# Kernel optimization log

Hardware: AMD Instinct MI355X
Metric: run time of the kernel (lower is better)

## Reference

```python
import jax, jax.numpy as jnp
import numpy as np

N_WIN = 7    # n_win hardcoded in AR_Attention
TOPK = 4     # topk routing windows
HEADS = 8    # num_heads


def setup_inputs() -> dict:
    key = jax.random.key(0)
    ks = jax.random.split(key, 6)
    B, H, W, C = 4, 56, 56, 256
    s = 0.02
    x = jax.random.normal(ks[0], (B, H, W, C), jnp.float32)
    Wqkv = jax.random.normal(ks[1], (C, 3 * C), jnp.float32) * s  # Linear(dim, 3*dim) (qk_dim=dim)
    bqkv = jnp.zeros((3 * C,), jnp.float32)
    Wo = jax.random.normal(ks[2], (C, C), jnp.float32) * s        # output projection Linear(dim, dim)
    bo = jnp.zeros((C,), jnp.float32)
    lepe_w = jax.random.normal(ks[3], (5, 5, 1, C), jnp.float32) * s  # 5x5 depthwise conv (side_dwconv=5)
    lepe_b = jnp.zeros((C,), jnp.float32)
    return {"x": x, "Wqkv": Wqkv, "bqkv": bqkv, "Wo": Wo, "bo": bo,
            "lepe_w": lepe_w, "lepe_b": lepe_b}


def reference(x, Wqkv, bqkv, Wo, bo, lepe_w, lepe_b):
    B, H, W, C = x.shape
    nw = N_WIN
    h, w = H // nw, W // nw           # region size (8x8)
    p2 = nw * nw                      # number of regions (49)
    hd = C // HEADS                   # head dim
    scale = float(C) ** -0.5          # qk_scale = qk_dim ** -0.5 (qk_dim = dim)

    # region partition: [B,H,W,C] -> [B,p2,h,w,C]
    xr = x.reshape(B, nw, h, nw, w, C).transpose(0, 1, 3, 2, 4, 5).reshape(B, p2, h, w, C)

    qkv = xr @ Wqkv + bqkv            # [B,p2,h,w,3C]
    q, kv = qkv[..., :C], qkv[..., C:]

    q_pix = q.reshape(B, p2, h * w, C)
    kv_pix = kv.reshape(B, p2, h * w, 2 * C)   # kv_downsample_mode='identity'

    # region-level queries/keys via per-window mean pooling
    q_win = q.mean((2, 3))                     # [B,p2,C]
    k_win = kv[..., :C].mean((2, 3))           # [B,p2,C]

    # LEPE: 5x5 depthwise conv on v over the full image grid
    v_img = kv[..., C:].reshape(B, nw, nw, h, w, C).transpose(0, 1, 3, 2, 4, 5).reshape(B, H, W, C)
    lepe = jax.lax.conv_general_dilated(
        v_img, lepe_w, (1, 1), 'SAME',
        dimension_numbers=('NHWC', 'HWIO', 'NHWC'),
        feature_group_count=C) + lepe_b

    # top-k window routing (param_routing=False, hard routing, mul_weight='none')
    r_logit = jnp.einsum('bpc,bqc->bpq', q_win * scale, k_win)  # [B,p2,p2]
    _, r_idx = jax.lax.top_k(r_logit, TOPK)                     # [B,p2,TOPK]

    # gather selected kv windows: [B,p2,TOPK,h*w,2C]
    kv_sel = jax.vmap(lambda kvp, i: kvp[i])(kv_pix, r_idx)

    k_sel = kv_sel[..., :C].reshape(B, p2, TOPK * h * w, HEADS, hd)
    v_sel = kv_sel[..., C:].reshape(B, p2, TOPK * h * w, HEADS, hd)
    qh = q_pix.reshape(B, p2, h * w, HEADS, hd)

    attn = jnp.einsum('bpqnd,bpknd->bpnqk', qh * scale, k_sel)  # [B,p2,heads,hw,TOPK*hw]
    attn = jax.nn.softmax(attn, axis=-1)
    out = jnp.einsum('bpnqk,bpknd->bpqnd', attn, v_sel).reshape(B, p2, h, w, C)

    # windows back to image grid
    out = out.reshape(B, nw, nw, h, w, C).transpose(0, 1, 3, 2, 4, 5).reshape(B, H, W, C)
    out = out + lepe
    return out @ Wo + bo
```

## Files before the change

### kernel.cpp

```cpp
#include <hip/hip_runtime.h>
#include <hip/hip_bf16.h>

#define NPIX 12544

typedef short bf16x8 __attribute__((ext_vector_type(8)));
typedef short bf16x4 __attribute__((ext_vector_type(4)));
typedef float f32x4  __attribute__((ext_vector_type(4)));

__device__ __forceinline__ float bf2f(unsigned short u) {
    unsigned int x = ((unsigned int)u) << 16;
    float f; __builtin_memcpy(&f, &x, sizeof(f)); return f;
}
__device__ __forceinline__ unsigned short f2bf(float f) {
    __hip_bfloat16 h = __float2bfloat16(f);
    unsigned short u; __builtin_memcpy(&u, &h, 2); return u;
}
__device__ __forceinline__ void load_lds16(const unsigned short* g, unsigned short* l) {
    __builtin_amdgcn_global_load_lds(
        (const __attribute__((address_space(1))) unsigned int*)g,
        (__attribute__((address_space(3))) unsigned int*)l,
        16, 0, 0);
}
__device__ __forceinline__ unsigned ldsoff(const void* p) {
    return (unsigned)(unsigned long long)(const __attribute__((address_space(3))) char*)p;
}
template<int OFF>
__device__ __forceinline__ bf16x4 tr16(unsigned addr) {
    bf16x4 d;
    asm volatile("ds_read_b64_tr_b16 %0, %1 offset:%c2"
                 : "=v"(d) : "v"(addr), "i"(OFF));
    return d;
}

__global__ __launch_bounds__(256) void k_prep(
    const float* __restrict__ X, unsigned short* __restrict__ Xb,
    float* __restrict__ xmean,
    const float* __restrict__ Wqkv, const float* __restrict__ Wo,
    unsigned short* __restrict__ Wtq, unsigned short* __restrict__ Wto)
{
    __shared__ __align__(16) unsigned char sm[64 * 65 * 4];
    const int t = threadIdx.x;
    const int blk = blockIdx.x;
    if (blk < 392) {
        float* part = (float*)sm;
        const int w = blk >> 1, hc = blk & 1;
        const int b = w / 49, p = w % 49;
        const int wi = p / 7, wj = p % 7;
        const int ch0 = hc * 128;
        const int ps = t >> 5, cg = t & 31;
        float4 s = {0.f, 0.f, 0.f, 0.f};
        #pragma unroll
        for (int i = 0; i < 8; i++) {
            int pp = ps * 8 + i;
            int y = wi * 8 + (pp >> 3), x = wj * 8 + (pp & 7);
            int idx = (((b * 56) + y) * 56 + x) * 256 + ch0 + cg * 4;
            float4 v = *reinterpret_cast<const float4*>(X + idx);
            s.x += v.x; s.y += v.y; s.z += v.z; s.w += v.w;
            ushort4 o = { f2bf(v.x), f2bf(v.y), f2bf(v.z), f2bf(v.w) };
            *reinterpret_cast<ushort4*>(Xb + idx) = o;
        }
        *reinterpret_cast<float4*>(part + t * 4) = *reinterpret_cast<float4*>(&s);
        __syncthreads();
        if (t < 32) {
            float4 m = {0.f, 0.f, 0.f, 0.f};
            #pragma unroll
            for (int ps2 = 0; ps2 < 8; ps2++) {
                float4 v = *reinterpret_cast<float4*>(part + (ps2 * 32 + t) * 4);
                m.x += v.x; m.y += v.y; m.z += v.z; m.w += v.w;
            }
            m.x *= (1.f / 64.f); m.y *= (1.f / 64.f);
            m.z *= (1.f / 64.f); m.w *= (1.f / 64.f);
            *reinterpret_cast<float4*>(xmean + w * 256 + ch0 + t * 4) = m;
        }
    } else {
        float* tile = (float*)sm;
        int tb = blk - 392;
        const float* Wsrc; unsigned short* Wdst; int N, kt, nt;
        if (tb < 48) { Wsrc = Wqkv; Wdst = Wtq; N = 768; kt = tb / 12; nt = tb % 12; }
        else { tb -= 48; Wsrc = Wo; Wdst = Wto; N = 256; kt = tb / 4; nt = tb % 4; }
        const int k0 = kt * 64, n0 = nt * 64;
        const int r0 = t >> 6, c = t & 63;
        #pragma unroll
        for (int i = 0; i < 16; i++) {
            int r = i * 4 + r0;
            tile[r * 65 + c] = Wsrc[(size_t)(k0 + r) * N + n0 + c];
        }
        __syncthreads();
        #pragma unroll
        for (int i = 0; i < 16; i++) {
            int n = i * 4 + r0;
            Wdst[(size_t)(n0 + n) * 256 + k0 + c] = f2bf(tile[c * 65 + n]);
        }
    }
}

__global__ __launch_bounds__(256) void k_main1(
    const unsigned short* __restrict__ A,
    const unsigned short* __restrict__ Bt,
    const float* __restrict__ bias,
    unsigned short* __restrict__ O,
    const float* __restrict__ xmean,
    const float* __restrict__ Wqkv,
    float* __restrict__ qwin, float* __restrict__ kwin)
{
    __shared__ __align__(16) unsigned char sm1[32768];
    const int t = threadIdx.x;
    const int blk = blockIdx.x;
    if (blk < 588) {
        unsigned short* As = (unsigned short*)sm1;
        unsigned short* Bs = (unsigned short*)(sm1 + 16384);
        const int m0 = (blk % 98) * 128, n0 = (blk / 98) * 128;
        const int wave = t >> 6, lane = t & 63, quad = lane >> 4, lo = lane & 15;
        const int wm = wave & 1, wn = wave >> 1;
        const int sr = wave * 16 + (lane >> 2);
        const int sc = lane & 3;
        f32x4 acc[4][4];
        #pragma unroll
        for (int i = 0; i < 4; i++)
            #pragma unroll
            for (int j = 0; j < 4; j++) acc[i][j] = (f32x4){0.f, 0.f, 0.f, 0.f};

        auto stage = [&](int it) {
            int kt = it * 32;
            unsigned short* Ad = As + (it & 1) * 4096;
            unsigned short* Bd = Bs + (it & 1) * 4096;
            #pragma unroll
            for (int j = 0; j < 2; j++) {
                int row = j * 64 + sr;
                int e = sc ^ ((row >> 1) & 3);
                load_lds16(A  + (size_t)(m0 + row) * 256 + kt + e * 8, &Ad[row * 32 + sc * 8]);
                load_lds16(Bt + (size_t)(n0 + row) * 256 + kt + e * 8, &Bd[row * 32 + sc * 8]);
            }
        };
        stage(0);
        for (int it = 0; it < 8; ++it) {
            if (it < 7) {
                stage(it + 1);
                asm volatile("s_waitcnt vmcnt(4)" ::: "memory");
            } else {
                asm volatile("s_waitcnt vmcnt(0)" ::: "memory");
            }
            __builtin_amdgcn_s_barrier();
            const unsigned short* Ac = As + (it & 1) * 4096;
            const unsigned short* Bc = Bs + (it & 1) * 4096;
            bf16x8 af[4], bfr[4];
            #pragma unroll
            for (int mt = 0; mt < 4; mt++) {
                int row = wm * 64 + mt * 16 + lo;
                int c = quad ^ ((row >> 1) & 3);
                af[mt] = *reinterpret_cast<const bf16x8*>(&Ac[row * 32 + c * 8]);
            }
            #pragma unroll
            for (int nt = 0; nt < 4; nt++) {
                int col = wn * 64 + nt * 16 + lo;
                int c = quad ^ ((col >> 1) & 3);
                bfr[nt] = *reinterpret_cast<const bf16x8*>(&Bc[col * 32 + c * 8]);
            }
            #pragma unroll
            for (int mt = 0; mt < 4; mt++)
                #pragma unroll
                for (int nt = 0; nt < 4; nt++)
                    acc[mt][nt] = __builtin_amdgcn_mfma_f32_16x16x32_bf16(
                        af[mt], bfr[nt], acc[mt][nt], 0, 0, 0);
            __builtin_amdgcn_s_barrier();
        }
        float bv[4];
        #pragma unroll
        for (int nt = 0; nt < 4; nt++) bv[nt] = bias[n0 + wn * 64 + nt * 16 + lo];
        #pragma unroll
        for (int mt = 0; mt < 4; mt++)
            #pragma unroll
            for (int nt = 0; nt < 4; nt++) {
                int n = n0 + wn * 64 + nt * 16 + lo;
                #pragma unroll
                for (int r = 0; r < 4; r++) {
                    int m = m0 + wm * 64 + mt * 16 + quad * 4 + r;
                    O[m * 768 + n] = f2bf(acc[mt][nt][r] + bv[nt]);
                }
            }
    } else {
        float* xs = (float*)sm1;
        const int u = blk - 588;
        const int bp = u % 196;
        const int half = u / 196;
        const int c = t;
        xs[c] = xmean[bp * 256 + c];
        __syncthreads();
        const int col = half * 256 + c;
        float a = 0.f;
        for (int k = 0; k < 256; k++) a += xs[k] * Wqkv[k * 768 + col];
        float* outp = half ? kwin : qwin;
        outp[bp * 256 + c] = a + bias[col];
    }
}

__global__ __launch_bounds__(256) void k_main2(
    const float* __restrict__ qwin, const float* __restrict__ kwin,
    int* __restrict__ ridx)
{
    __shared__ __align__(16) unsigned char sm2[1024];
    const int t = threadIdx.x;
    const int blk = blockIdx.x;
    float* part = (float*)sm2;
    float* lg   = (float*)(sm2 + 49 * 4 * 4);
    const int b = blk / 49, p = blk % 49;
    if (t < 196) {
        int d = t >> 2, pr = t & 3;
        const float* qp = &qwin[(b * 49 + p) * 256];
        const float* kp = &kwin[(b * 49 + d) * 256];
        float a = 0.f;
        for (int ch = pr * 64; ch < pr * 64 + 64; ch++) a += qp[ch] * kp[ch];
        part[d * 4 + pr] = a;
    }
    __syncthreads();
    if (t < 49) lg[t] = part[t * 4 + 0] + part[t * 4 + 1] + part[t * 4 + 2] + part[t * 4 + 3];
    __syncthreads();
    if (t == 0) {
        unsigned long long used = 0ull;
        for (int sel = 0; sel < 4; sel++) {
            float best = -1e30f; int bi = 0;
            for (int qq = 0; qq < 49; qq++)
                if (!((used >> qq) & 1ull) && lg[qq] > best) { best = lg[qq]; bi = qq; }
            used |= (1ull << bi);
            ridx[blk * 4 + sel] = bi;
        }
    }
}

__global__ __launch_bounds__(256) void k_attn(
    const unsigned short* __restrict__ QKV,
    const int* __restrict__ ridx,
    const float* __restrict__ lw, const float* __restrict__ lb,
    unsigned short* __restrict__ Osum)
{
    __shared__ __align__(16) unsigned char smem[40064];
    unsigned short* Vs  = (unsigned short*)smem;
    unsigned short* Ks  = (unsigned short*)(smem + 16384);
    unsigned short* PST = (unsigned short*)(smem + 16384);
    float* lws          = (float*)(smem + 36864);

    const int p = blockIdx.x, head = blockIdx.y, b = blockIdx.z;
    const int t = threadIdx.x;
    const int wi = p / 7, wj = p % 7;
    const int wave = t >> 6, lane = t & 63, quad = lane >> 4, lo = lane & 15;
    const int pix4 = t >> 2, c4 = t & 3;

    const int q  = wave * 16 + lo;
    const int qy = wi * 8 + (q >> 3), qx = wj * 8 + (q & 7);

    bf16x8 af = *reinterpret_cast<const bf16x8*>(
        QKV + (size_t)(((b * 56) + qy) * 56 + qx) * 768 + head * 32 + quad * 8);

    if (t < 200) {
        int tap = t >> 3, ci = (t & 7) * 4;
        *reinterpret_cast<float4*>(&lws[tap * 32 + ci]) =
            *reinterpret_cast<const float4*>(lw + tap * 256 + head * 32 + ci);
    }
    {
        const int4 rs = *reinterpret_cast<const int4*>(&ridx[(b * 49 + p) * 4]);
        const int sels[4] = { rs.x, rs.y, rs.z, rs.w };
        #pragma unroll
        for (int pass = 0; pass < 4; pass++) {
            int sel = sels[pass];
            int si = sel / 7, sj = sel % 7;
            int y = si * 8 + (pix4 >> 3), x = sj * 8 + (pix4 & 7);
            const unsigned short* base = QKV + (((b * 56) + y) * 56 + x) * 768 + 256 + head * 32;
            bf16x8 kv = *reinterpret_cast<const bf16x8*>(base + c4 * 8);
            bf16x8 vv = *reinterpret_cast<const bf16x8*>(base + 256 + c4 * 8);
            int krow = pass * 64 + pix4;
            int sw = c4 ^ ((krow >> 3) & 3);
            *reinterpret_cast<bf16x8*>(&Ks[krow * 40 + sw * 8]) = kv;
            *reinterpret_cast<bf16x8*>(
                &Vs[(krow >> 2) * 128 + (c4 >> 1) * 64 + (krow & 3) * 16 + (c4 & 1) * 8]) = vv;
        }
    }
    __syncthreads();

    float lep[8];
    {
        float4 b0 = *reinterpret_cast<const float4*>(lb + head * 32 + quad * 8);
        float4 b1 = *reinterpret_cast<const float4*>(lb + head * 32 + quad * 8 + 4);
        lep[0] = b0.x; lep[1] = b0.y; lep[2] = b0.z; lep[3] = b0.w;
        lep[4] = b1.x; lep[5] = b1.y; lep[6] = b1.z; lep[7] = b1.w;
        #pragma unroll
        for (int ky = 0; ky < 5; ky++) {
            int yy = qy + ky - 2;
            int yc = min(max(yy, 0), 55);
            bool yin = (yy >= 0) & (yy < 56);
            #pragma unroll
            for (int kx = 0; kx < 5; kx++) {
                int xx = qx + kx - 2;
                int xc = min(max(xx, 0), 55);
                float mf = (yin & (xx >= 0) & (xx < 56)) ? 1.f : 0.f;
                bf16x8 v = *reinterpret_cast<const bf16x8*>(
                    QKV + (size_t)(((b * 56) + yc) * 56 + xc) * 768 + 512 + head * 32 + quad * 8);
                const float* wrow = &lws[(ky * 5 + kx) * 32 + quad * 8];
                float4 w0 = *reinterpret_cast<const float4*>(wrow);
                float4 w1 = *reinterpret_cast<const float4*>(wrow + 4);
                lep[0] += bf2f((unsigned short)v[0]) * w0.x * mf;
                lep[1] += bf2f((unsigned short)v[1]) * w0.y * mf;
                lep[2] += bf2f((unsigned short)v[2]) * w0.z * mf;
                lep[3] += bf2f((unsigned short)v[3]) * w0.w * mf;
                lep[4] += bf2f((unsigned short)v[4]) * w1.x * mf;
                lep[5] += bf2f((unsigned short)v[5]) * w1.y * mf;
                lep[6] += bf2f((unsigned short)v[6]) * w1.z * mf;
                lep[7] += bf2f((unsigned short)v[7]) * w1.w * mf;
            }
        }
    }

    f32x4 sc[16];
    {
        f32x4 z = (f32x4){0.f, 0.f, 0.f, 0.f};
        #pragma unroll
        for (int nt = 0; nt < 16; nt++) {
            int key = nt * 16 + lo;
            bf16x8 bfr = *reinterpret_cast<const bf16x8*>(
                &Ks[key * 40 + ((quad ^ ((key >> 3) & 3)) * 8)]);
            sc[nt] = __builtin_amdgcn_mfma_f32_16x16x32_bf16(af, bfr, z, 0, 0, 0);
        }
    }
    float M[4] = {-1e30f, -1e30f, -1e30f, -1e30f};
    #pragma unroll
    for (int nt = 0; nt < 16; nt++)
        #pragma unroll
        for (int r = 0; r < 4; r++) M[r] = fmaxf(M[r], sc[nt][r] * 0.0625f);
    #pragma unroll
    for (int d = 1; d < 16; d <<= 1)
        #pragma unroll
        for (int r = 0; r < 4; r++) M[r] = fmaxf(M[r], __shfl_xor(M[r], d));
    float l[4] = {0.f, 0.f, 0.f, 0.f};
    #pragma unroll
    for (int nt = 0; nt < 16; nt++)
        #pragma unroll
        for (int r = 0; r < 4; r++) {
            float e = __expf(sc[nt][r] * 0.0625f - M[r]);
            sc[nt][r] = e;
            l[r] += e;
        }
    #pragma unroll
    for (int d = 1; d < 16; d <<= 1)
        #pragma unroll
        for (int r = 0; r < 4; r++) l[r] += __shfl_xor(l[r], d);

    __syncthreads();

    unsigned short* myP = PST + wave * 2048;
    const unsigned pbase = ldsoff(myP) + quad * 256 + lo * 8;
    const unsigned vbase = ldsoff(Vs)  + quad * 512 + lo * 8;
    f32x4 o0 = (f32x4){0.f, 0.f, 0.f, 0.f}, o1 = o0;
    #pragma unroll
    for (int h = 0; h < 2; h++) {
        #pragma unroll
        for (int nt2 = 0; nt2 < 8; nt2++) {
            int nt = h * 8 + nt2;
            ushort4 pk = { f2bf(sc[nt][0]), f2bf(sc[nt][1]),
                           f2bf(sc[nt][2]), f2bf(sc[nt][3]) };
            *reinterpret_cast<ushort4*>(&myP[(nt2 * 16 + lo) * 16 + quad * 4]) = pk;
        }
        asm volatile("s_waitcnt lgkmcnt(0)" ::: "memory");
        __builtin_amdgcn_sched_barrier(0);

        const unsigned vb = vbase + h * 8192;
        bf16x4 ra0, ra1, rw00, rw01, rw10, rw11;
        ra0  = tr16<0>(pbase);
        ra1  = tr16<128>(pbase);
        rw00 = tr16<0>(vb);
        rw01 = tr16<256>(vb);
        rw10 = tr16<128>(vb);
        rw11 = tr16<384>(vb);
        #pragma unroll
        for (int kt = 0; kt < 4; kt++) {
            bf16x4 na0, na1, nw00, nw01, nw10, nw11;
            if (kt < 3) {
                unsigned pn = pbase + (kt + 1) * 1024;
                unsigned vn = vb + (kt + 1) * 2048;
                na0  = tr16<0>(pn);
                na1  = tr16<128>(pn);
                nw00 = tr16<0>(vn);
                nw01 = tr16<256>(vn);
                nw10 = tr16<128>(vn);
                nw11 = tr16<384>(vn);
                asm volatile("s_waitcnt lgkmcnt(6)" ::: "memory");
            } else {
                asm volatile("s_waitcnt lgkmcnt(0)" ::: "memory");
            }
            __builtin_amdgcn_sched_barrier(0);
            bf16x8 pa, vb0, vb1;
            #pragma unroll
            for (int j = 0; j < 4; j++) {
                pa[j]  = ra0[j];  pa[4 + j]  = ra1[j];
                vb0[j] = rw00[j]; vb0[4 + j] = rw01[j];
                vb1[j] = rw10[j]; vb1[4 + j] = rw11[j];
            }
            o0 = __builtin_amdgcn_mfma_f32_16x16x32_bf16(pa, vb0, o0, 0, 0, 0);
            o1 = __builtin_amdgcn_mfma_f32_16x16x32_bf16(pa, vb1, o1, 0, 0, 0);
            if (kt < 3) { ra0 = na0; ra1 = na1; rw00 = nw00; rw01 = nw01; rw10 = nw10; rw11 = nw11; }
        }
    }

    {
        float i0 = 1.f / l[0], i1 = 1.f / l[1], i2 = 1.f / l[2], i3 = 1.f / l[3];
        ushort4 p0 = { f2bf(o0[0] * i0), f2bf(o0[1] * i1),
                       f2bf(o0[2] * i2), f2bf(o0[3] * i3) };
        ushort4 p1 = { f2bf(o1[0] * i0), f2bf(o1[1] * i1),
                       f2bf(o1[2] * i2), f2bf(o1[3] * i3) };
        *reinterpret_cast<ushort4*>(&myP[lo * 16 + quad * 4]) = p0;
        *reinterpret_cast<ushort4*>(&myP[(16 + lo) * 16 + quad * 4]) = p1;
    }
    const unsigned oaddr = ldsoff(myP) + quad * 256 + lo * 8;
    asm volatile("s_waitcnt lgkmcnt(0)" ::: "memory");
    __builtin_amdgcn_sched_barrier(0);
    bf16x4 e0 = tr16<0>(oaddr);
    bf16x4 e1 = tr16<128>(oaddr);
    asm volatile("s_waitcnt lgkmcnt(0)" ::: "memory");
    __builtin_amdgcn_sched_barrier(0);
    {
        size_t gbase = (size_t)(((b * 56) + qy) * 56 + qx) * 256 + head * 32 + quad * 8;
        bf16x8 oo;
        #pragma unroll
        for (int j = 0; j < 4; j++) {
            oo[j]     = (short)f2bf(bf2f((unsigned short)e0[j]) + lep[j]);
            oo[4 + j] = (short)f2bf(bf2f((unsigned short)e1[j]) + lep[4 + j]);
        }
        *reinterpret_cast<bf16x8*>(Osum + gbase) = oo;
    }
}

__global__ __launch_bounds__(256) void k_proj(
    const unsigned short* __restrict__ A,
    const unsigned short* __restrict__ Bt,
    const float* __restrict__ bias,
    float* __restrict__ O)
{
    __shared__ __align__(16) unsigned short As[2 * 128 * 32];
    __shared__ __align__(16) unsigned short Bs[2 * 64 * 32];
    const int t = threadIdx.x;
    const int m0 = blockIdx.x * 128, n0 = blockIdx.y * 64;
    const int wave = t >> 6, lane = t & 63, quad = lane >> 4, lo = lane & 15;
    const int sr = wave * 16 + (lane >> 2);
    const int sc = lane & 3;
    f32x4 acc[2][4];
    #pragma unroll
    for (int i = 0; i < 2; i++)
        #pragma unroll
        for (int j = 0; j < 4; j++) acc[i][j] = (f32x4){0.f, 0.f, 0.f, 0.f};

    auto stage = [&](int it) {
        int kt = it * 32;
        unsigned short* Ad = As + (it & 1) * 4096;
        unsigned short* Bd = Bs + (it & 1) * 2048;
        #pragma unroll
        for (int j = 0; j < 2; j++) {
            int row = j * 64 + sr;
            int e = sc ^ ((row >> 1) & 3);
            load_lds16(A + (size_t)(m0 + row) * 256 + kt + e * 8, &Ad[row * 32 + sc * 8]);
        }
        {
            int e = sc ^ ((sr >> 1) & 3);
            load_lds16(Bt + (size_t)(n0 + sr) * 256 + kt + e * 8, &Bd[sr * 32 + sc * 8]);
        }
    };
    stage(0);
    for (int it = 0; it < 8; ++it) {
        if (it < 7) {
            stage(it + 1);
            asm volatile("s_waitcnt vmcnt(3)" ::: "memory");
        } else {
            asm volatile("s_waitcnt vmcnt(0)" ::: "memory");
        }
        __builtin_amdgcn_s_barrier();
        const unsigned short* Ac = As + (it & 1) * 4096;
        const unsigned short* Bc = Bs + (it & 1) * 2048;
        bf16x8 af[2], bfr[4];
        #pragma unroll
        for (int mt = 0; mt < 2; mt++) {
            int row = wave * 32 + mt * 16 + lo;
            int c = quad ^ ((row >> 1) & 3);
            af[mt] = *reinterpret_cast<const bf16x8*>(&Ac[row * 32 + c * 8]);
        }
        #pragma unroll
        for (int nt = 0; nt < 4; nt++) {
            int col = nt * 16 + lo;
            int c = quad ^ ((col >> 1) & 3);
            bfr[nt] = *reinterpret_cast<const bf16x8*>(&Bc[col * 32 + c * 8]);
        }
        #pragma unroll
        for (int mt = 0; mt < 2; mt++)
            #pragma unroll
            for (int nt = 0; nt < 4; nt++)
                acc[mt][nt] = __builtin_amdgcn_mfma_f32_16x16x32_bf16(
                    af[mt], bfr[nt], acc[mt][nt], 0, 0, 0);
        __builtin_amdgcn_s_barrier();
    }
    float bv[4];
    #pragma unroll
    for (int nt = 0; nt < 4; nt++) bv[nt] = bias[n0 + nt * 16 + lo];
    #pragma unroll
    for (int mt = 0; mt < 2; mt++)
        #pragma unroll
        for (int nt = 0; nt < 4; nt++) {
            int n = n0 + nt * 16 + lo;
            #pragma unroll
            for (int r = 0; r < 4; r++) {
                int m = m0 + wave * 32 + mt * 16 + quad * 4 + r;
                O[m * 256 + n] = acc[mt][nt][r] + bv[nt];
            }
        }
}

extern "C" void kernel_launch(void* const* d_in, const int* in_sizes, int n_in,
                              void* d_out, int out_size, void* d_ws, size_t ws_size,
                              hipStream_t stream)
{
    const float* x    = (const float*)d_in[0];
    const float* Wqkv = (const float*)d_in[1];
    const float* bqkv = (const float*)d_in[2];
    const float* Wo   = (const float*)d_in[3];
    const float* bo   = (const float*)d_in[4];
    const float* lw   = (const float*)d_in[5];
    const float* lb   = (const float*)d_in[6];
    float* out = (float*)d_out;

    char* ws = (char*)d_ws;
    size_t off = 0;
    unsigned short* qkv   = (unsigned short*)(ws + off); off += (size_t)NPIX * 768 * 2;
    unsigned short* xb    = (unsigned short*)(ws + off); off += (size_t)NPIX * 256 * 2;
    unsigned short* Wtq   = (unsigned short*)(ws + off); off += 768 * 256 * 2;
    unsigned short* Wto   = (unsigned short*)(ws + off); off += 256 * 256 * 2;
    unsigned short* Osum  = (unsigned short*)(ws + off); off += (size_t)NPIX * 256 * 2;
    float* xmean = (float*)(ws + off); off += 196 * 256 * 4;
    float* qwin  = (float*)(ws + off); off += 196 * 256 * 4;
    float* kwin  = (float*)(ws + off); off += 196 * 256 * 4;
    int*   ridx  = (int*)(ws + off);   off += 196 * 4 * 4;

    k_prep <<<dim3(456),      256, 0, stream>>>(x, xb, xmean, Wqkv, Wo, Wtq, Wto);
    k_main1<<<dim3(980),      256, 0, stream>>>(xb, Wtq, bqkv, qkv, xmean, Wqkv, qwin, kwin);
    k_main2<<<dim3(196),      256, 0, stream>>>(qwin, kwin, ridx);
    k_attn <<<dim3(49, 8, 4), 256, 0, stream>>>(qkv, ridx, lw, lb, Osum);
    k_proj <<<dim3(98, 4),    256, 0, stream>>>(Osum, Wto, bo, out);
}
```

Before: 178.2 us.

## Recompute QK scores in chunked PV loop to drop score registers and P buffer

Restructures the attention kernel into two passes. The first pass computes QK^T only to get the row max. The second pass recomputes scores two tiles at a time, exponentiates them, stages them through a small per-wave LDS buffer and immediately runs the PV MFMA. This removes the 16-tile score array held in registers and the block-wide sync, and moves the P staging buffer so it no longer aliases K. The aim is lower VGPR pressure and better occupancy, at the cost of running the QK MFMAs twice. K also loses its padded, swizzled layout, which may cause LDS bank conflicts, and the software prefetch of V/P tiles is gone.

```diff
diff --git a/kernel.cpp b/kernel.cpp
--- a/kernel.cpp
+++ b/kernel.cpp
@@ -236,7 +236,7 @@
     __shared__ __align__(16) unsigned char smem[40064];
     unsigned short* Vs  = (unsigned short*)smem;
     unsigned short* Ks  = (unsigned short*)(smem + 16384);
-    unsigned short* PST = (unsigned short*)(smem + 16384);
+    unsigned short* PST = (unsigned short*)(smem + 32768);
     float* lws          = (float*)(smem + 36864);
 
     const int p = blockIdx.x, head = blockIdx.y, b = blockIdx.z;
@@ -268,8 +268,7 @@
             bf16x8 kv = *reinterpret_cast<const bf16x8*>(base + c4 * 8);
             bf16x8 vv = *reinterpret_cast<const bf16x8*>(base + 256 + c4 * 8);
             int krow = pass * 64 + pix4;
-            int sw = c4 ^ ((krow >> 3) & 3);
-            *reinterpret_cast<bf16x8*>(&Ks[krow * 40 + sw * 8]) = kv;
+            *reinterpret_cast<bf16x8*>(&Ks[krow * 32 + c4 * 8]) = kv;
             *reinterpret_cast<bf16x8*>(
                 &Vs[(krow >> 2) * 128 + (c4 >> 1) * 64 + (krow & 3) * 16 + (c4 & 1) * 8]) = vv;
         }
@@ -309,95 +308,68 @@
         }
     }
 
-    f32x4 sc[16];
-    {
-        f32x4 z = (f32x4){0.f, 0.f, 0.f, 0.f};
-        #pragma unroll
-        for (int nt = 0; nt < 16; nt++) {
-            int key = nt * 16 + lo;
-            bf16x8 bfr = *reinterpret_cast<const bf16x8*>(
-                &Ks[key * 40 + ((quad ^ ((key >> 3) & 3)) * 8)]);
-            sc[nt] = __builtin_amdgcn_mfma_f32_16x16x32_bf16(af, bfr, z, 0, 0, 0);
-        }
-    }
+    const f32x4 z = (f32x4){0.f, 0.f, 0.f, 0.f};
+
     float M[4] = {-1e30f, -1e30f, -1e30f, -1e30f};
-    #pragma unroll
-    for (int nt = 0; nt < 16; nt++)
-        #pragma unroll
-        for (int r = 0; r < 4; r++) M[r] = fmaxf(M[r], sc[nt][r] * 0.0625f);
+    #pragma unroll 4
+    for (int nt = 0; nt < 16; nt++) {
+        bf16x8 bfr = *reinterpret_cast<const bf16x8*>(&Ks[(nt * 16 + lo) * 32 + quad * 8]);
+        f32x4 s = __builtin_amdgcn_mfma_f32_16x16x32_bf16(af, bfr, z, 0, 0, 0);
+        #pragma unroll
+        for (int r = 0; r < 4; r++) M[r] = fmaxf(M[r], s[r] * 0.0625f);
+    }
     #pragma unroll
     for (int d = 1; d < 16; d <<= 1)
         #pragma unroll
         for (int r = 0; r < 4; r++) M[r] = fmaxf(M[r], __shfl_xor(M[r], d));
+
+    unsigned short* myP = PST + wave * 512;
+    const unsigned pbase = ldsoff(myP) + quad * 256 + lo * 8;
+    const unsigned vbase = ldsoff(Vs)  + quad * 512 + lo * 8;
     float l[4] = {0.f, 0.f, 0.f, 0.f};
-    #pragma unroll
-    for (int nt = 0; nt < 16; nt++)
+    f32x4 o0 = z, o1 = z;
+    for (int c = 0; c < 8; c++) {
+        bf16x8 k0 = *reinterpret_cast<const bf16x8*>(&Ks[((2 * c) * 16 + lo) * 32 + quad * 8]);
+        bf16x8 k1 = *reinterpret_cast<const bf16x8*>(&Ks[((2 * c + 1) * 16 + lo) * 32 + quad * 8]);
+        f32x4 s0 = __builtin_amdgcn_mfma_f32_16x16x32_bf16(af, k0, z, 0, 0, 0);
+        f32x4 s1 = __builtin_amdgcn_mfma_f32_16x16x32_bf16(af, k1, z, 0, 0, 0);
+        float e0[4], e1[4];
         #pragma unroll
         for (int r = 0; r < 4; r++) {
-            float e = __expf(sc[nt][r] * 0.0625f - M[r]);
-            sc[nt][r] = e;
-            l[r] += e;
-        }
+            e0[r] = __expf(s0[r] * 0.0625f - M[r]);
+            e1[r] = __expf(s1[r] * 0.0625f - M[r]);
+            l[r] += e0[r] + e1[r];
+        }
+        ushort4 p0 = { f2bf(e0[0]), f2bf(e0[1]), f2bf(e0[2]), f2bf(e0[3]) };
+        ushort4 p1 = { f2bf(e1[0]), f2bf(e1[1]), f2bf(e1[2]), f2bf(e1[3]) };
+        *reinterpret_cast<ushort4*>(&myP[lo * 16 + quad * 4]) = p0;
+        *reinterpret_cast<ushort4*>(&myP[(16 + lo) * 16 + quad * 4]) = p1;
+        asm volatile("s_waitcnt lgkmcnt(0)" ::: "memory");
+        __builtin_amdgcn_sched_barrier(0);
+
+        const unsigned vb = vbase + c * 2048;
+        bf16x4 ra0  = tr16<0>(pbase);
+        bf16x4 ra1  = tr16<128>(pbase);
+        bf16x4 rw00 = tr16<0>(vb);
+        bf16x4 rw01 = tr16<256>(vb);
+        bf16x4 rw10 = tr16<128>(vb);
+        bf16x4 rw11 = tr16<384>(vb);
+        asm volatile("s_waitcnt lgkmcnt(0)" ::: "memory");
+        __builtin_amdgcn_sched_barrier(0);
+        bf16x8 pa, vb0, vb1;
+        #pragma unroll
+        for (int j = 0; j < 4; j++) {
+            pa[j]  = ra0[j];  pa[4 + j]  = ra1[j];
+            vb0[j] = rw00[j]; vb0[4 + j] = rw01[j];
+            vb1[j] = rw10[j]; vb1[4 + j] = rw11[j];
+        }
+        o0 = __builtin_amdgcn_mfma_f32_16x16x32_bf16(pa, vb0, o0, 0, 0, 0);
+        o1 = __builtin_amdgcn_mfma_f32_16x16x32_bf16(pa, vb1, o1, 0, 0, 0);
+    }
     #pragma unroll
     for (int d = 1; d < 16; d <<= 1)
         #pragma unroll
         for (int r = 0; r < 4; r++) l[r] += __shfl_xor(l[r], d);
-
-    __syncthreads();
-
-    unsigned short* myP = PST + wave * 2048;
-    const unsigned pbase = ldsoff(myP) + quad * 256 + lo * 8;
-    const unsigned vbase = ldsoff(Vs)  + quad * 512 + lo * 8;
-    f32x4 o0 = (f32x4){0.f, 0.f, 0.f, 0.f}, o1 = o0;
-    #pragma unroll
-    for (int h = 0; h < 2; h++) {
-        #pragma unroll
-        for (int nt2 = 0; nt2 < 8; nt2++) {
-            int nt = h * 8 + nt2;
-            ushort4 pk = { f2bf(sc[nt][0]), f2bf(sc[nt][1]),
-                           f2bf(sc[nt][2]), f2bf(sc[nt][3]) };
-            *reinterpret_cast<ushort4*>(&myP[(nt2 * 16 + lo) * 16 + quad * 4]) = pk;
-        }
-        asm volatile("s_waitcnt lgkmcnt(0)" ::: "memory");
-        __builtin_amdgcn_sched_barrier(0);
-
-        const unsigned vb = vbase + h * 8192;
-        bf16x4 ra0, ra1, rw00, rw01, rw10, rw11;
-        ra0  = tr16<0>(pbase);
-        ra1  = tr16<128>(pbase);
-        rw00 = tr16<0>(vb);
-        rw01 = tr16<256>(vb);
-        rw10 = tr16<128>(vb);
-        rw11 = tr16<384>(vb);
-        #pragma unroll
-        for (int kt = 0; kt < 4; kt++) {
-            bf16x4 na0, na1, nw00, nw01, nw10, nw11;
-            if (kt < 3) {
-                unsigned pn = pbase + (kt + 1) * 1024;
-                unsigned vn = vb + (kt + 1) * 2048;
-                na0  = tr16<0>(pn);
-                na1  = tr16<128>(pn);
-                nw00 = tr16<0>(vn);
-                nw01 = tr16<256>(vn);
-                nw10 = tr16<128>(vn);
-                nw11 = tr16<384>(vn);
-                asm volatile("s_waitcnt lgkmcnt(6)" ::: "memory");
-            } else {
-                asm volatile("s_waitcnt lgkmcnt(0)" ::: "memory");
-            }
-            __builtin_amdgcn_sched_barrier(0);
-            bf16x8 pa, vb0, vb1;
-            #pragma unroll
-            for (int j = 0; j < 4; j++) {
-                pa[j]  = ra0[j];  pa[4 + j]  = ra1[j];
-                vb0[j] = rw00[j]; vb0[4 + j] = rw01[j];
-                vb1[j] = rw10[j]; vb1[4 + j] = rw11[j];
-            }
-            o0 = __builtin_amdgcn_mfma_f32_16x16x32_bf16(pa, vb0, o0, 0, 0, 0);
-            o1 = __builtin_amdgcn_mfma_f32_16x16x32_bf16(pa, vb1, o1, 0, 0, 0);
-            if (kt < 3) { ra0 = na0; ra1 = na1; rw00 = nw00; rw01 = nw01; rw10 = nw10; rw11 = nw11; }
-        }
-    }
 
     {
         float i0 = 1.f / l[0], i1 = 1.f / l[1], i2 = 1.f / l[2], i3 = 1.f / l[3];
```

After: 181.2 us. Within noise of the previous version (+1.7%).
